# Optimization experiments

Hardware: AMD Instinct MI355X
Metric: run time of the kernel (lower is better)

## Reference

```python
import jax, jax.numpy as jnp
import numpy as np

D_MODEL = 1024
N_HEADS = 16
N_KV = 4
HEAD_DIM = D_MODEL // N_HEADS
B, T, CACHE_LEN = 2, 1024, 1024
MAX_SEQ = 4096
ROPE_BASE = 10000.0


def _rope_tables(max_seq_len=MAX_SEQ, head_dim=HEAD_DIM, base=ROPE_BASE):
    inv_freq = 1.0 / (base ** (np.arange(0, head_dim, 2, dtype=np.float32) / head_dim))
    t = np.arange(max_seq_len, dtype=np.float32)
    freqs = np.outer(t, inv_freq)                      # [S, hd/2]
    emb = np.concatenate([freqs, freqs], axis=-1)      # [S, hd]
    return jnp.asarray(np.cos(emb)), jnp.asarray(np.sin(emb))


def _rotate_half(x):
    x1, x2 = jnp.split(x, 2, axis=-1)
    return jnp.concatenate([-x2, x1], axis=-1)


def setup_inputs() -> dict:
    key = jax.random.key(0)
    ks = jax.random.split(key, 8)
    return {
        "x": jax.random.normal(ks[0], (B, T, D_MODEL), dtype=jnp.float32),
        "k_cache": jax.random.normal(ks[1], (B, N_KV, CACHE_LEN, HEAD_DIM), dtype=jnp.float32),
        "v_cache": jax.random.normal(ks[2], (B, N_KV, CACHE_LEN, HEAD_DIM), dtype=jnp.float32),
        "position_indices": jax.random.randint(ks[3], (B, T), 0, 1024, dtype=jnp.int32),
        "Wq": jax.random.normal(ks[4], (D_MODEL, D_MODEL), dtype=jnp.float32) * 0.02,
        "Wk": jax.random.normal(ks[5], (D_MODEL, N_KV * HEAD_DIM), dtype=jnp.float32) * 0.02,
        "Wv": jax.random.normal(ks[6], (D_MODEL, N_KV * HEAD_DIM), dtype=jnp.float32) * 0.02,
        "Wo": jax.random.normal(ks[7], (D_MODEL, D_MODEL), dtype=jnp.float32) * 0.02,
    }


def reference(x, k_cache, v_cache, position_indices, Wq, Wk, Wv, Wo):
    Bq, Tq, C = x.shape
    n_kv, cache_len, hd = k_cache.shape[1], k_cache.shape[2], k_cache.shape[3]
    n_heads = Wq.shape[1] // hd
    n_rep = n_heads // n_kv
    scale = hd ** -0.5

    cos, sin = _rope_tables()

    # projections -> [B, H, T, hd]
    q = (x @ Wq).reshape(Bq, Tq, n_heads, hd).transpose(0, 2, 1, 3)
    k = (x @ Wk).reshape(Bq, Tq, n_kv, hd).transpose(0, 2, 1, 3)
    v = (x @ Wv).reshape(Bq, Tq, n_kv, hd).transpose(0, 2, 1, 3)

    # progress-aware RoPE: position-indexed gather into tables, offset by cache len
    offset = cache_len
    t_seq = jnp.arange(Tq, dtype=jnp.int32)[None, :] + offset          # [1, T]
    idx = jnp.clip(position_indices.astype(jnp.int32) + t_seq, 0, cos.shape[0] - 1)  # [B, T]
    cos_b = cos[idx][:, None]  # [B, 1, T, hd]
    sin_b = sin[idx][:, None]
    q = q * cos_b + _rotate_half(q) * sin_b
    k = k * cos_b + _rotate_half(k) * sin_b

    # KV-cache concat
    k = jnp.concatenate([k_cache, k], axis=2)  # [B, n_kv, S, hd]
    v = jnp.concatenate([v_cache, v], axis=2)

    # GQA head expansion (repeat each kv head n_rep times, contiguous grouping)
    k_exp = jnp.repeat(k, n_rep, axis=1)  # [B, H, S, hd]
    v_exp = jnp.repeat(v, n_rep, axis=1)

    # manual attention path (k_cache provided -> NO causal mask, matching torch code)
    attn = jnp.einsum("bhtd,bhsd->bhts", q, k_exp) * scale
    attn = jax.nn.softmax(attn, axis=-1)
    out = jnp.einsum("bhts,bhsd->bhtd", attn, v_exp)
    out = out.transpose(0, 2, 1, 3).reshape(Bq, Tq, C)
    return out @ Wo, k, v
```

## Files before the change

kernel.cpp:

```cpp
#include <hip/hip_runtime.h>
#include <hip/hip_bf16.h>
#include <stdint.h>

#define D_MODEL 1024
#define N_HEADS 16
#define N_KV 4
#define HD 64
#define BB 2
#define TT 1024
#define CACHE_LEN 1024
#define SS 2048
#define MAX_SEQ 4096
#define QKV_N 1536
#define NROWS 32768
#define GRP_EL (SS * HD)
#define NSP 2

typedef __attribute__((ext_vector_type(8))) short bf16x8;
typedef __attribute__((ext_vector_type(4))) float f32x4;

__device__ inline short f2bs(float f) {
    __hip_bfloat16 h = __float2bfloat16(f);
    return *reinterpret_cast<short*>(&h);
}
__device__ inline float bs2f(short s) {
    return __uint_as_float((unsigned)(unsigned short)s << 16);
}

__device__ inline int kfrag_off(int s, int d) {
    return (s >> 4) * 1024 + ((d >= 32) ? 512 : 0) + ((((d & 31) >> 3) * 16 + (s & 15)) * 8) + (d & 7);
}
__device__ inline int vfrag_off(int s, int d) {
    return ((s >> 5) * 4 + (d >> 4)) * 512 + ((((s >> 2) & 3) * 16 + (d & 15)) * 8)
         + (((s >> 4) & 1) * 4) + (s & 3);
}

__device__ void transp_body(const float* __restrict__ src, short* __restrict__ dst,
                            int N, int bx, int by) {
    __shared__ short tile[32][34];
    int tx = threadIdx.x & 31, ty = threadIdx.x >> 5;
    int n0 = bx * 32, k0 = by * 32;
#pragma unroll
    for (int i = 0; i < 4; i++)
        tile[ty + i * 8][tx] = f2bs(src[(size_t)(k0 + ty + i * 8) * N + n0 + tx]);
    __syncthreads();
#pragma unroll
    for (int i = 0; i < 4; i++)
        dst[(size_t)(n0 + ty + i * 8) * 1024 + k0 + tx] = tile[tx][ty + i * 8];
}

__global__ void k_prep(const float* __restrict__ x, short* __restrict__ xb,
                       const float* __restrict__ Wq, const float* __restrict__ Wk,
                       const float* __restrict__ Wv, const float* __restrict__ Wo,
                       short* __restrict__ Wt, short* __restrict__ Wot,
                       const float* __restrict__ k_cache, const float* __restrict__ v_cache,
                       float* __restrict__ k_out, float* __restrict__ v_out,
                       short* __restrict__ kf, short* __restrict__ vf,
                       const int* __restrict__ pos,
                       float* __restrict__ costab, float* __restrict__ sintab) {
    int id = blockIdx.x;
    int g = threadIdx.x;
    if (id < 2048) {
        int i = (id * 256 + g) * 4;
        float4 v = *reinterpret_cast<const float4*>(x + i);
        short4 o = make_short4(f2bs(v.x), f2bs(v.y), f2bs(v.z), f2bs(v.w));
        *reinterpret_cast<short4*>(xb + i) = o;
        return;
    }
    id -= 2048;
    if (id < 1024) { transp_body(Wq, Wt, 1024, id & 31, id >> 5); return; }
    id -= 1024;
    if (id < 256)  { transp_body(Wk, Wt + (size_t)1024 * 1024, 256, id & 7, id >> 3); return; }
    id -= 256;
    if (id < 256)  { transp_body(Wv, Wt + (size_t)1280 * 1024, 256, id & 7, id >> 3); return; }
    id -= 256;
    if (id < 1024) { transp_body(Wo, Wot, 1024, id & 31, id >> 5); return; }
    id -= 1024;
    if (id < 2048) {
        int i = id * 256 + g;
        int d = i & 63;
        int s = (i >> 6) & 1023;
        int bh = i >> 16;
        size_t cidx = ((size_t)bh * CACHE_LEN + s) * HD + d;
        size_t oidx = ((size_t)bh * SS + s) * HD + d;
        float kv = k_cache[cidx];
        float vv = v_cache[cidx];
        k_out[oidx] = kv;
        v_out[oidx] = vv;
        kf[(size_t)bh * GRP_EL + kfrag_off(s, d)] = f2bs(kv);
        vf[(size_t)bh * GRP_EL + vfrag_off(s, d)] = f2bs(vv);
        return;
    }
    id -= 2048;
    {
        int p = id * 256 + g;
        int row = p >> 5, i = p & 31;
        int idx = pos[row] + (row & 1023) + CACHE_LEN;
        idx = min(max(idx, 0), MAX_SEQ - 1);
        float inv = expf(-(float)i * (9.210340371976184f / 32.0f));
        float sv, cv;
        sincosf((float)idx * inv, &sv, &cv);
        costab[p] = cv;
        sintab[p] = sv;
    }
}

__global__ __launch_bounds__(256) void k_gemm_qkv(
    const short* __restrict__ A, const short* __restrict__ Bt,
    const float* __restrict__ costab, const float* __restrict__ sintab,
    short* __restrict__ qb, short* __restrict__ kf, short* __restrict__ vf,
    float* __restrict__ k_out, float* __restrict__ v_out) {
    __shared__ float eplds[64 * 65];
    short* sA = (short*)eplds;
    short* sB = sA + 4096;
    int m0 = blockIdx.y * 64, n0 = blockIdx.x * 64;
    int g = threadIdx.x;
    int lane = g & 63, wave = g >> 6;
    int wr = wave >> 1, wc = wave & 1;
    int quad = lane >> 4, l15 = lane & 15;

    f32x4 acc[2][2] = {};

    for (int k0 = 0; k0 < 1024; k0 += 64) {
        __syncthreads();
#pragma unroll
        for (int i = 0; i < 2; i++) {
            int cb = wave * 2 + i;
            int h = cb >> 2, c = cb & 3;
            int row = c * 16 + (lane >> 2);
            int kcol = k0 + h * 32 + (lane & 3) * 8;
            const short* srcA = A + (size_t)(m0 + row) * 1024 + kcol;
            const short* srcB = Bt + (size_t)(n0 + row) * 1024 + kcol;
            __builtin_amdgcn_global_load_lds(
                (const __attribute__((address_space(1))) void*)srcA,
                (__attribute__((address_space(3))) void*)((char*)sA + h * 4096 + c * 1024), 16, 0, 0);
            __builtin_amdgcn_global_load_lds(
                (const __attribute__((address_space(1))) void*)srcB,
                (__attribute__((address_space(3))) void*)((char*)sB + h * 4096 + c * 1024), 16, 0, 0);
        }
        __syncthreads();
#pragma unroll
        for (int h = 0; h < 2; h++) {
            bf16x8 af[2], bfr[2];
#pragma unroll
            for (int i = 0; i < 2; i++)
                af[i] = *reinterpret_cast<const bf16x8*>(sA + h * 2048 + (wr * 32 + i * 16 + l15) * 32 + quad * 8);
#pragma unroll
            for (int j = 0; j < 2; j++)
                bfr[j] = *reinterpret_cast<const bf16x8*>(sB + h * 2048 + (wc * 32 + j * 16 + l15) * 32 + quad * 8);
#pragma unroll
            for (int i = 0; i < 2; i++)
#pragma unroll
                for (int j = 0; j < 2; j++)
                    acc[i][j] = __builtin_amdgcn_mfma_f32_16x16x32_bf16(af[i], bfr[j], acc[i][j], 0, 0, 0);
        }
    }
    __syncthreads();
#pragma unroll
    for (int i = 0; i < 2; i++)
#pragma unroll
        for (int j = 0; j < 2; j++)
#pragma unroll
            for (int r = 0; r < 4; r++)
                eplds[(wr * 32 + i * 16 + quad * 4 + r) * 65 + wc * 32 + j * 16 + l15] = acc[i][j][r];
    __syncthreads();

    int bx = blockIdx.x;
    const float QS = 0.18033688011112042f;
    if (bx < 20) {
#pragma unroll
        for (int rep = 0; rep < 8; rep++) {
            int p = rep * 256 + g;
            int row = p >> 5, i = p & 31;
            int m = m0 + row;
            int b = m >> 10, t = m & 1023;
            float cv = costab[m * 32 + i], sv = sintab[m * 32 + i];
            float x1 = eplds[row * 65 + i], x2 = eplds[row * 65 + i + 32];
            float o1 = x1 * cv - x2 * sv;
            float o2 = x2 * cv + x1 * sv;
            if (bx < 16) {
                size_t qbase = ((size_t)(b * N_HEADS + bx) * TT + t) * HD;
                qb[qbase + i]      = f2bs(o1 * QS);
                qb[qbase + i + 32] = f2bs(o2 * QS);
            } else {
                int h = bx - 16;
                int s = CACHE_LEN + t;
                size_t kbase = ((size_t)(b * N_KV + h) * SS + s) * HD;
                k_out[kbase + i]      = o1;
                k_out[kbase + i + 32] = o2;
                short* kfb = kf + (size_t)(b * N_KV + h) * GRP_EL;
                kfb[kfrag_off(s, i)]      = f2bs(o1);
                kfb[kfrag_off(s, i + 32)] = f2bs(o2);
            }
        }
    } else {
        int h = bx - 20;
#pragma unroll
        for (int rep = 0; rep < 16; rep++) {
            int p = rep * 256 + g;
            int row = p >> 6, d = p & 63;
            int m = m0 + row;
            int b = m >> 10, t = m & 1023;
            int s = CACHE_LEN + t;
            float val = eplds[row * 65 + d];
            v_out[((size_t)(b * N_KV + h) * SS + s) * HD + d] = val;
            vf[(size_t)(b * N_KV + h) * GRP_EL + vfrag_off(s, d)] = f2bs(val);
        }
    }
}

__global__ __launch_bounds__(256) void k_gemm64(
    const short* __restrict__ A, const short* __restrict__ Bt, float* __restrict__ C,
    int M, int N, int K) {
    __shared__ short sA[2][64 * 32];
    __shared__ short sB[2][64 * 32];
    int m0 = blockIdx.y * 64, n0 = blockIdx.x * 64;
    int g = threadIdx.x;
    int lane = g & 63, wave = g >> 6;
    int wr = wave >> 1, wc = wave & 1;
    int quad = lane >> 4, l15 = lane & 15;

    f32x4 acc[2][2] = {};

    for (int k0 = 0; k0 < K; k0 += 64) {
        __syncthreads();
#pragma unroll
        for (int i = 0; i < 2; i++) {
            int cb = wave * 2 + i;
            int h = cb >> 2, c = cb & 3;
            int row = c * 16 + (lane >> 2);
            int kcol = k0 + h * 32 + (lane & 3) * 8;
            const short* srcA = A + (size_t)(m0 + row) * K + kcol;
            const short* srcB = Bt + (size_t)(n0 + row) * K + kcol;
            __builtin_amdgcn_global_load_lds(
                (const __attribute__((address_space(1))) void*)srcA,
                (__attribute__((address_space(3))) void*)((char*)&sA[h][0] + c * 1024), 16, 0, 0);
            __builtin_amdgcn_global_load_lds(
                (const __attribute__((address_space(1))) void*)srcB,
                (__attribute__((address_space(3))) void*)((char*)&sB[h][0] + c * 1024), 16, 0, 0);
        }
        __syncthreads();
#pragma unroll
        for (int h = 0; h < 2; h++) {
            bf16x8 af[2], bfr[2];
#pragma unroll
            for (int i = 0; i < 2; i++)
                af[i] = *reinterpret_cast<const bf16x8*>(&sA[h][(wr * 32 + i * 16 + l15) * 32 + quad * 8]);
#pragma unroll
            for (int j = 0; j < 2; j++)
                bfr[j] = *reinterpret_cast<const bf16x8*>(&sB[h][(wc * 32 + j * 16 + l15) * 32 + quad * 8]);
#pragma unroll
            for (int i = 0; i < 2; i++)
#pragma unroll
                for (int j = 0; j < 2; j++)
                    acc[i][j] = __builtin_amdgcn_mfma_f32_16x16x32_bf16(af[i], bfr[j], acc[i][j], 0, 0, 0);
        }
    }
#pragma unroll
    for (int i = 0; i < 2; i++) {
        int m = m0 + wr * 32 + i * 16 + quad * 4;
#pragma unroll
        for (int j = 0; j < 2; j++) {
            int n = n0 + wc * 32 + j * 16 + l15;
#pragma unroll
            for (int r = 0; r < 4; r++)
                C[(size_t)(m + r) * N + n] = acc[i][j][r];
        }
    }
}

__global__ __launch_bounds__(256, 4) void k_attn(
    const short* __restrict__ qb, const short* __restrict__ kf, const short* __restrict__ vf,
    ushort* __restrict__ po, float* __restrict__ pl) {
    __shared__ short tile[8192];
    int bx = blockIdx.x;
    int sp = bx >> 5;
    int bh = bx & 31;
    int b = bh >> 4, h = bh & 15;
    int hkv = h >> 2;
    int lane = threadIdx.x & 63, wave = threadIdx.x >> 6;
    int quad = lane >> 4, l15 = lane & 15;
    int tw0 = blockIdx.y * 128 + wave * 16;
    int tw1 = tw0 + 64;

    const short* qrow0 = qb + ((size_t)bh * TT + tw0 + l15) * HD;
    const short* qrow1 = qb + ((size_t)bh * TT + tw1 + l15) * HD;
    bf16x8 aq00 = *reinterpret_cast<const bf16x8*>(qrow0 + quad * 8);
    bf16x8 aq01 = *reinterpret_cast<const bf16x8*>(qrow0 + 32 + quad * 8);
    bf16x8 aq10 = *reinterpret_cast<const bf16x8*>(qrow1 + quad * 8);
    bf16x8 aq11 = *reinterpret_cast<const bf16x8*>(qrow1 + 32 + quad * 8);

    const short* kfb = kf + (size_t)(b * N_KV + hkv) * GRP_EL;
    const short* vfb = vf + (size_t)(b * N_KV + hkv) * GRP_EL;

    f32x4 o0[4] = {}, o1[4] = {};
    float lr0 = 0.f, lr1 = 0.f;

    int sbeg = sp * (SS / NSP);
    for (int s0 = sbeg; s0 < sbeg + SS / NSP; s0 += 64) {
        __syncthreads();
#pragma unroll
        for (int i = 0; i < 4; i++) {
            int ch = wave * 4 + i;
            const short* src = (ch < 8)
                ? kfb + (s0 >> 4) * 1024 + ch * 512 + lane * 8
                : vfb + (s0 >> 5) * 2048 + (ch - 8) * 512 + lane * 8;
            __builtin_amdgcn_global_load_lds(
                (const __attribute__((address_space(1))) void*)src,
                (__attribute__((address_space(3))) void*)((char*)tile + ch * 1024), 16, 0, 0);
        }
        __syncthreads();

#pragma unroll
        for (int pp = 0; pp < 2; pp++) {
            f32x4 s0c[2], s1c[2];
#pragma unroll
            for (int ti = 0; ti < 2; ti++) {
                int nt = pp * 2 + ti;
                bf16x8 ak0 = *reinterpret_cast<const bf16x8*>(tile + nt * 1024 + lane * 8);
                bf16x8 ak1 = *reinterpret_cast<const bf16x8*>(tile + nt * 1024 + 512 + lane * 8);
                f32x4 z = {};
                z = __builtin_amdgcn_mfma_f32_16x16x32_bf16(ak0, aq00, z, 0, 0, 0);
                z = __builtin_amdgcn_mfma_f32_16x16x32_bf16(ak1, aq01, z, 0, 0, 0);
                s0c[ti] = z;
                f32x4 w = {};
                w = __builtin_amdgcn_mfma_f32_16x16x32_bf16(ak0, aq10, w, 0, 0, 0);
                w = __builtin_amdgcn_mfma_f32_16x16x32_bf16(ak1, aq11, w, 0, 0, 0);
                s1c[ti] = w;
            }
            bf16x8 bp0, bp1;
#pragma unroll
            for (int ti = 0; ti < 2; ti++)
#pragma unroll
                for (int r = 0; r < 4; r++) {
                    float p0 = exp2f(s0c[ti][r]);
                    float p1 = exp2f(s1c[ti][r]);
                    lr0 += p0;
                    lr1 += p1;
                    bp0[ti * 4 + r] = f2bs(p0);
                    bp1[ti * 4 + r] = f2bs(p1);
                }
#pragma unroll
            for (int dt = 0; dt < 4; dt++) {
                bf16x8 av = *reinterpret_cast<const bf16x8*>(
                    tile + 4096 + (pp * 4 + dt) * 512 + lane * 8);
                o0[dt] = __builtin_amdgcn_mfma_f32_16x16x32_bf16(av, bp0, o0[dt], 0, 0, 0);
                o1[dt] = __builtin_amdgcn_mfma_f32_16x16x32_bf16(av, bp1, o1[dt], 0, 0, 0);
            }
        }
    }

    lr0 += __shfl_xor(lr0, 16);
    lr0 += __shfl_xor(lr0, 32);
    lr1 += __shfl_xor(lr1, 16);
    lr1 += __shfl_xor(lr1, 32);

    size_t row0 = (size_t)bh * TT + tw0 + l15;
    size_t row1 = (size_t)bh * TT + tw1 + l15;
    if (quad == 0) {
        pl[(size_t)sp * NROWS + row0] = lr0;
        pl[(size_t)sp * NROWS + row1] = lr1;
    }
#pragma unroll
    for (int dt = 0; dt < 4; dt++) {
        ushort4 w0, w1;
        w0.x = (ushort)f2bs(o0[dt][0]); w0.y = (ushort)f2bs(o0[dt][1]);
        w0.z = (ushort)f2bs(o0[dt][2]); w0.w = (ushort)f2bs(o0[dt][3]);
        w1.x = (ushort)f2bs(o1[dt][0]); w1.y = (ushort)f2bs(o1[dt][1]);
        w1.z = (ushort)f2bs(o1[dt][2]); w1.w = (ushort)f2bs(o1[dt][3]);
        *reinterpret_cast<ushort4*>(po + ((size_t)sp * NROWS + row0) * 64 + dt * 16 + quad * 4) = w0;
        *reinterpret_cast<ushort4*>(po + ((size_t)sp * NROWS + row1) * 64 + dt * 16 + quad * 4) = w1;
    }
}

__global__ void k_merge(const ushort* __restrict__ po, const float* __restrict__ pl,
                        short* __restrict__ ob) {
    int g = threadIdx.x;
    int row = blockIdx.x * 16 + (g >> 4);
    int d0 = (g & 15) * 4;
    float l = 0.f;
#pragma unroll
    for (int sp = 0; sp < NSP; sp++) l += pl[(size_t)sp * NROWS + row];
    float a0 = 0, a1 = 0, a2 = 0, a3 = 0;
#pragma unroll
    for (int sp = 0; sp < NSP; sp++) {
        ushort4 u = *reinterpret_cast<const ushort4*>(po + ((size_t)sp * NROWS + row) * 64 + d0);
        a0 += __uint_as_float((unsigned)u.x << 16);
        a1 += __uint_as_float((unsigned)u.y << 16);
        a2 += __uint_as_float((unsigned)u.z << 16);
        a3 += __uint_as_float((unsigned)u.w << 16);
    }
    float inv = 1.0f / l;
    int bh = row >> 10, t = row & 1023;
    int b = bh >> 4, h = bh & 15;
    short4 w = make_short4(f2bs(a0 * inv), f2bs(a1 * inv), f2bs(a2 * inv), f2bs(a3 * inv));
    *reinterpret_cast<short4*>(ob + (size_t)(b * TT + t) * D_MODEL + h * 64 + d0) = w;
}

extern "C" void kernel_launch(void* const* d_in, const int* in_sizes, int n_in,
                              void* d_out, int out_size, void* d_ws, size_t ws_size,
                              hipStream_t stream) {
    (void)in_sizes; (void)n_in; (void)out_size; (void)ws_size;
    const float* x       = (const float*)d_in[0];
    const float* k_cache = (const float*)d_in[1];
    const float* v_cache = (const float*)d_in[2];
    const int*   pos     = (const int*)d_in[3];
    const float* Wq      = (const float*)d_in[4];
    const float* Wk      = (const float*)d_in[5];
    const float* Wv      = (const float*)d_in[6];
    const float* Wo      = (const float*)d_in[7];

    float* out   = (float*)d_out;
    float* k_out = out + (size_t)BB * TT * D_MODEL;
    float* v_out = k_out + (size_t)BB * N_KV * SS * HD;

    char* ws = (char*)d_ws;
    short* xb     = (short*)(ws);
    short* Wt     = (short*)(ws + (4u << 20));
    float* costab = (float*)(ws + (7u << 20));
    float* sintab = (float*)(ws + (7u << 20) + (256u << 10));
    short* qbuf   = (short*)(ws + (8u << 20));
    short* kfr    = (short*)(ws + (12u << 20));
    short* vfr    = (short*)(ws + (14u << 20));
    short* obuf   = (short*)(ws + (16u << 20));
    short* Wot    = (short*)(ws + (20u << 20));
    float* pl     = (float*)(ws + (22u << 20));
    ushort* po    = (ushort*)(ws);

    k_prep<<<6912, 256, 0, stream>>>(x, xb, Wq, Wk, Wv, Wo, Wt, Wot,
                                     k_cache, v_cache, k_out, v_out, kfr, vfr,
                                     pos, costab, sintab);

    k_gemm_qkv<<<dim3(QKV_N / 64, 2048 / 64), 256, 0, stream>>>(
        xb, Wt, costab, sintab, qbuf, kfr, vfr, k_out, v_out);

    k_attn<<<dim3(32 * NSP, TT / 128), 256, 0, stream>>>(qbuf, kfr, vfr, po, pl);
    k_merge<<<2048, 256, 0, stream>>>(po, pl, obuf);

    k_gemm64<<<dim3(1024 / 64, 2048 / 64), 256, 0, stream>>>(
        obuf, Wot, (float*)d_out, 2048, 1024, 1024);
}
```

Before: 149.4 us.

## Double-buffer LDS staging in GEMMs and attention, drop split-KV merge

Adds double-buffered LDS staging to the QKV GEMM, the output GEMM and the attention kernel, so the global-to-LDS copy of the next K/KV tile is issued before computing on the current tile. Each loop now needs one barrier per iteration instead of two. The attention kernel no longer splits the sequence into two halves with a separate merge kernel; it processes the full sequence per block and normalises and writes bf16 output directly. This removes a launch and the partial-result round trip, but halves the attention grid (256 blocks) and doubles LDS use per block, which may cut occupancy.

```diff
diff --git a/kernel.cpp b/kernel.cpp
--- a/kernel.cpp
+++ b/kernel.cpp
@@ -12,9 +12,7 @@
 #define SS 2048
 #define MAX_SEQ 4096
 #define QKV_N 1536
-#define NROWS 32768
 #define GRP_EL (SS * HD)
-#define NSP 2
 
 typedef __attribute__((ext_vector_type(8))) short bf16x8;
 typedef __attribute__((ext_vector_type(4))) float f32x4;
@@ -23,9 +21,10 @@
     __hip_bfloat16 h = __float2bfloat16(f);
     return *reinterpret_cast<short*>(&h);
 }
-__device__ inline float bs2f(short s) {
-    return __uint_as_float((unsigned)(unsigned short)s << 16);
-}
+
+#define GLDS(gp, lp) __builtin_amdgcn_global_load_lds( \
+    (const __attribute__((address_space(1))) void*)(gp), \
+    (__attribute__((address_space(3))) void*)(lp), 16, 0, 0)
 
 __device__ inline int kfrag_off(int s, int d) {
     return (s >> 4) * 1024 + ((d >= 32) ? 512 : 0) + ((((d & 31) >> 3) * 16 + (s & 15)) * 8) + (d & 7);
@@ -110,9 +109,10 @@
     const float* __restrict__ costab, const float* __restrict__ sintab,
     short* __restrict__ qb, short* __restrict__ kf, short* __restrict__ vf,
     float* __restrict__ k_out, float* __restrict__ v_out) {
-    __shared__ float eplds[64 * 65];
-    short* sA = (short*)eplds;
-    short* sB = sA + 4096;
+    __shared__ short smem[16384];
+    short* sA = smem;
+    short* sB = smem + 8192;
+    float* eplds = (float*)smem;
     int m0 = blockIdx.y * 64, n0 = blockIdx.x * 64;
     int g = threadIdx.x;
     int lane = g & 63, wave = g >> 6;
@@ -121,41 +121,48 @@
 
     f32x4 acc[2][2] = {};
 
+    int srow = (lane >> 2);
+    int scol = (lane & 3) * 8;
+#define STAGE_G(buf, k0)                                                              \
+    {                                                                                 \
+        _Pragma("unroll")                                                             \
+        for (int i = 0; i < 2; i++) {                                                 \
+            int cb = wave * 2 + i;                                                    \
+            int h = cb >> 2, c = cb & 3;                                              \
+            int row = c * 16 + srow;                                                  \
+            int kcol = (k0) + h * 32 + scol;                                          \
+            GLDS(A + (size_t)(m0 + row) * 1024 + kcol,                                \
+                 (char*)(sA + (buf) * 4096 + h * 2048) + c * 1024);                   \
+            GLDS(Bt + (size_t)(n0 + row) * 1024 + kcol,                               \
+                 (char*)(sB + (buf) * 4096 + h * 2048) + c * 1024);                   \
+        }                                                                             \
+    }
+
+    STAGE_G(0, 0);
+    __syncthreads();
+    int buf = 0;
     for (int k0 = 0; k0 < 1024; k0 += 64) {
-        __syncthreads();
-#pragma unroll
-        for (int i = 0; i < 2; i++) {
-            int cb = wave * 2 + i;
-            int h = cb >> 2, c = cb & 3;
-            int row = c * 16 + (lane >> 2);
-            int kcol = k0 + h * 32 + (lane & 3) * 8;
-            const short* srcA = A + (size_t)(m0 + row) * 1024 + kcol;
-            const short* srcB = Bt + (size_t)(n0 + row) * 1024 + kcol;
-            __builtin_amdgcn_global_load_lds(
-                (const __attribute__((address_space(1))) void*)srcA,
-                (__attribute__((address_space(3))) void*)((char*)sA + h * 4096 + c * 1024), 16, 0, 0);
-            __builtin_amdgcn_global_load_lds(
-                (const __attribute__((address_space(1))) void*)srcB,
-                (__attribute__((address_space(3))) void*)((char*)sB + h * 4096 + c * 1024), 16, 0, 0);
-        }
-        __syncthreads();
+        if (k0 + 64 < 1024) STAGE_G(buf ^ 1, k0 + 64);
 #pragma unroll
         for (int h = 0; h < 2; h++) {
             bf16x8 af[2], bfr[2];
 #pragma unroll
             for (int i = 0; i < 2; i++)
-                af[i] = *reinterpret_cast<const bf16x8*>(sA + h * 2048 + (wr * 32 + i * 16 + l15) * 32 + quad * 8);
+                af[i] = *reinterpret_cast<const bf16x8*>(
+                    sA + buf * 4096 + h * 2048 + (wr * 32 + i * 16 + l15) * 32 + quad * 8);
 #pragma unroll
             for (int j = 0; j < 2; j++)
-                bfr[j] = *reinterpret_cast<const bf16x8*>(sB + h * 2048 + (wc * 32 + j * 16 + l15) * 32 + quad * 8);
+                bfr[j] = *reinterpret_cast<const bf16x8*>(
+                    sB + buf * 4096 + h * 2048 + (wc * 32 + j * 16 + l15) * 32 + quad * 8);
 #pragma unroll
             for (int i = 0; i < 2; i++)
 #pragma unroll
                 for (int j = 0; j < 2; j++)
                     acc[i][j] = __builtin_amdgcn_mfma_f32_16x16x32_bf16(af[i], bfr[j], acc[i][j], 0, 0, 0);
         }
-    }
-    __syncthreads();
+        __syncthreads();
+        buf ^= 1;
+    }
 #pragma unroll
     for (int i = 0; i < 2; i++)
 #pragma unroll
@@ -212,8 +219,8 @@
 __global__ __launch_bounds__(256) void k_gemm64(
     const short* __restrict__ A, const short* __restrict__ Bt, float* __restrict__ C,
     int M, int N, int K) {
-    __shared__ short sA[2][64 * 32];
-    __shared__ short sB[2][64 * 32];
+    __shared__ short sA[2][2][2048];
+    __shared__ short sB[2][2][2048];
     int m0 = blockIdx.y * 64, n0 = blockIdx.x * 64;
     int g = threadIdx.x;
     int lane = g & 63, wave = g >> 6;
@@ -221,40 +228,42 @@
     int quad = lane >> 4, l15 = lane & 15;
 
     f32x4 acc[2][2] = {};
-
+    int srow = (lane >> 2);
+    int scol = (lane & 3) * 8;
+#define STAGE_W(buf, k0)                                                             \
+    {                                                                                \
+        _Pragma("unroll")                                                            \
+        for (int i = 0; i < 2; i++) {                                                \
+            int cb = wave * 2 + i;                                                   \
+            int h = cb >> 2, c = cb & 3;                                             \
+            int row = c * 16 + srow;                                                 \
+            int kcol = (k0) + h * 32 + scol;                                         \
+            GLDS(A + (size_t)(m0 + row) * K + kcol, (char*)&sA[buf][h][0] + c * 1024);\
+            GLDS(Bt + (size_t)(n0 + row) * K + kcol, (char*)&sB[buf][h][0] + c * 1024);\
+        }                                                                            \
+    }
+    STAGE_W(0, 0);
+    __syncthreads();
+    int buf = 0;
     for (int k0 = 0; k0 < K; k0 += 64) {
-        __syncthreads();
-#pragma unroll
-        for (int i = 0; i < 2; i++) {
-            int cb = wave * 2 + i;
-            int h = cb >> 2, c = cb & 3;
-            int row = c * 16 + (lane >> 2);
-            int kcol = k0 + h * 32 + (lane & 3) * 8;
-            const short* srcA = A + (size_t)(m0 + row) * K + kcol;
-            const short* srcB = Bt + (size_t)(n0 + row) * K + kcol;
-            __builtin_amdgcn_global_load_lds(
-                (const __attribute__((address_space(1))) void*)srcA,
-                (__attribute__((address_space(3))) void*)((char*)&sA[h][0] + c * 1024), 16, 0, 0);
-            __builtin_amdgcn_global_load_lds(
-                (const __attribute__((address_space(1))) void*)srcB,
-                (__attribute__((address_space(3))) void*)((char*)&sB[h][0] + c * 1024), 16, 0, 0);
-        }
-        __syncthreads();
+        if (k0 + 64 < K) STAGE_W(buf ^ 1, k0 + 64);
 #pragma unroll
         for (int h = 0; h < 2; h++) {
             bf16x8 af[2], bfr[2];
 #pragma unroll
             for (int i = 0; i < 2; i++)
-                af[i] = *reinterpret_cast<const bf16x8*>(&sA[h][(wr * 32 + i * 16 + l15) * 32 + quad * 8]);
+                af[i] = *reinterpret_cast<const bf16x8*>(&sA[buf][h][(wr * 32 + i * 16 + l15) * 32 + quad * 8]);
 #pragma unroll
             for (int j = 0; j < 2; j++)
-                bfr[j] = *reinterpret_cast<const bf16x8*>(&sB[h][(wc * 32 + j * 16 + l15) * 32 + quad * 8]);
+                bfr[j] = *reinterpret_cast<const bf16x8*>(&sB[buf][h][(wc * 32 + j * 16 + l15) * 32 + quad * 8]);
 #pragma unroll
             for (int i = 0; i < 2; i++)
 #pragma unroll
                 for (int j = 0; j < 2; j++)
                     acc[i][j] = __builtin_amdgcn_mfma_f32_16x16x32_bf16(af[i], bfr[j], acc[i][j], 0, 0, 0);
         }
+        __syncthreads();
+        buf ^= 1;
     }
 #pragma unroll
     for (int i = 0; i < 2; i++) {
@@ -271,11 +280,9 @@
 
 __global__ __launch_bounds__(256, 4) void k_attn(
     const short* __restrict__ qb, const short* __restrict__ kf, const short* __restrict__ vf,
-    ushort* __restrict__ po, float* __restrict__ pl) {
-    __shared__ short tile[8192];
-    int bx = blockIdx.x;
-    int sp = bx >> 5;
-    int bh = bx & 31;
+    short* __restrict__ ob) {
+    __shared__ short tile[2][8192];
+    int bh = blockIdx.x;
     int b = bh >> 4, h = bh & 15;
     int hkv = h >> 2;
     int lane = threadIdx.x & 63, wave = threadIdx.x >> 6;
@@ -296,29 +303,32 @@
     f32x4 o0[4] = {}, o1[4] = {};
     float lr0 = 0.f, lr1 = 0.f;
 
-    int sbeg = sp * (SS / NSP);
-    for (int s0 = sbeg; s0 < sbeg + SS / NSP; s0 += 64) {
-        __syncthreads();
-#pragma unroll
-        for (int i = 0; i < 4; i++) {
-            int ch = wave * 4 + i;
-            const short* src = (ch < 8)
-                ? kfb + (s0 >> 4) * 1024 + ch * 512 + lane * 8
-                : vfb + (s0 >> 5) * 2048 + (ch - 8) * 512 + lane * 8;
-            __builtin_amdgcn_global_load_lds(
-                (const __attribute__((address_space(1))) void*)src,
-                (__attribute__((address_space(3))) void*)((char*)tile + ch * 1024), 16, 0, 0);
-        }
-        __syncthreads();
-
+#define STAGE_KV(bufi, s0)                                                    \
+    {                                                                         \
+        _Pragma("unroll")                                                     \
+        for (int i = 0; i < 4; i++) {                                         \
+            int ch = wave * 4 + i;                                            \
+            const short* src = (ch < 8)                                       \
+                ? kfb + ((s0) >> 4) * 1024 + ch * 512 + lane * 8              \
+                : vfb + ((s0) >> 5) * 2048 + (ch - 8) * 512 + lane * 8;       \
+            GLDS(src, (char*)&tile[bufi][0] + ch * 1024);                     \
+        }                                                                     \
+    }
+
+    STAGE_KV(0, 0);
+    __syncthreads();
+    int buf = 0;
+    for (int s0 = 0; s0 < SS; s0 += 64) {
+        if (s0 + 64 < SS) STAGE_KV(buf ^ 1, s0 + 64);
+        const short* tb = &tile[buf][0];
 #pragma unroll
         for (int pp = 0; pp < 2; pp++) {
             f32x4 s0c[2], s1c[2];
 #pragma unroll
             for (int ti = 0; ti < 2; ti++) {
                 int nt = pp * 2 + ti;
-                bf16x8 ak0 = *reinterpret_cast<const bf16x8*>(tile + nt * 1024 + lane * 8);
-                bf16x8 ak1 = *reinterpret_cast<const bf16x8*>(tile + nt * 1024 + 512 + lane * 8);
+                bf16x8 ak0 = *reinterpret_cast<const bf16x8*>(tb + nt * 1024 + lane * 8);
+                bf16x8 ak1 = *reinterpret_cast<const bf16x8*>(tb + nt * 1024 + 512 + lane * 8);
                 f32x4 z = {};
                 z = __builtin_amdgcn_mfma_f32_16x16x32_bf16(ak0, aq00, z, 0, 0, 0);
                 z = __builtin_amdgcn_mfma_f32_16x16x32_bf16(ak1, aq01, z, 0, 0, 0);
@@ -343,58 +353,33 @@
 #pragma unroll
             for (int dt = 0; dt < 4; dt++) {
                 bf16x8 av = *reinterpret_cast<const bf16x8*>(
-                    tile + 4096 + (pp * 4 + dt) * 512 + lane * 8);
+                    tb + 4096 + (pp * 4 + dt) * 512 + lane * 8);
                 o0[dt] = __builtin_amdgcn_mfma_f32_16x16x32_bf16(av, bp0, o0[dt], 0, 0, 0);
                 o1[dt] = __builtin_amdgcn_mfma_f32_16x16x32_bf16(av, bp1, o1[dt], 0, 0, 0);
             }
         }
+        __syncthreads();
+        buf ^= 1;
     }
 
     lr0 += __shfl_xor(lr0, 16);
     lr0 += __shfl_xor(lr0, 32);
     lr1 += __shfl_xor(lr1, 16);
     lr1 += __shfl_xor(lr1, 32);
-
-    size_t row0 = (size_t)bh * TT + tw0 + l15;
-    size_t row1 = (size_t)bh * TT + tw1 + l15;
-    if (quad == 0) {
-        pl[(size_t)sp * NROWS + row0] = lr0;
-        pl[(size_t)sp * NROWS + row1] = lr1;
-    }
+    float inv0 = 1.0f / lr0;
+    float inv1 = 1.0f / lr1;
+
+    size_t row0 = (size_t)(b * TT) + tw0 + l15;
+    size_t row1 = (size_t)(b * TT) + tw1 + l15;
 #pragma unroll
     for (int dt = 0; dt < 4; dt++) {
-        ushort4 w0, w1;
-        w0.x = (ushort)f2bs(o0[dt][0]); w0.y = (ushort)f2bs(o0[dt][1]);
-        w0.z = (ushort)f2bs(o0[dt][2]); w0.w = (ushort)f2bs(o0[dt][3]);
-        w1.x = (ushort)f2bs(o1[dt][0]); w1.y = (ushort)f2bs(o1[dt][1]);
-        w1.z = (ushort)f2bs(o1[dt][2]); w1.w = (ushort)f2bs(o1[dt][3]);
-        *reinterpret_cast<ushort4*>(po + ((size_t)sp * NROWS + row0) * 64 + dt * 16 + quad * 4) = w0;
-        *reinterpret_cast<ushort4*>(po + ((size_t)sp * NROWS + row1) * 64 + dt * 16 + quad * 4) = w1;
-    }
-}
-
-__global__ void k_merge(const ushort* __restrict__ po, const float* __restrict__ pl,
-                        short* __restrict__ ob) {
-    int g = threadIdx.x;
-    int row = blockIdx.x * 16 + (g >> 4);
-    int d0 = (g & 15) * 4;
-    float l = 0.f;
-#pragma unroll
-    for (int sp = 0; sp < NSP; sp++) l += pl[(size_t)sp * NROWS + row];
-    float a0 = 0, a1 = 0, a2 = 0, a3 = 0;
-#pragma unroll
-    for (int sp = 0; sp < NSP; sp++) {
-        ushort4 u = *reinterpret_cast<const ushort4*>(po + ((size_t)sp * NROWS + row) * 64 + d0);
-        a0 += __uint_as_float((unsigned)u.x << 16);
-        a1 += __uint_as_float((unsigned)u.y << 16);
-        a2 += __uint_as_float((unsigned)u.z << 16);
-        a3 += __uint_as_float((unsigned)u.w << 16);
-    }
-    float inv = 1.0f / l;
-    int bh = row >> 10, t = row & 1023;
-    int b = bh >> 4, h = bh & 15;
-    short4 w = make_short4(f2bs(a0 * inv), f2bs(a1 * inv), f2bs(a2 * inv), f2bs(a3 * inv));
-    *reinterpret_cast<short4*>(ob + (size_t)(b * TT + t) * D_MODEL + h * 64 + d0) = w;
+        short4 w0 = make_short4(f2bs(o0[dt][0] * inv0), f2bs(o0[dt][1] * inv0),
+                                f2bs(o0[dt][2] * inv0), f2bs(o0[dt][3] * inv0));
+        short4 w1 = make_short4(f2bs(o1[dt][0] * inv1), f2bs(o1[dt][1] * inv1),
+                                f2bs(o1[dt][2] * inv1), f2bs(o1[dt][3] * inv1));
+        *reinterpret_cast<short4*>(ob + row0 * D_MODEL + h * 64 + dt * 16 + quad * 4) = w0;
+        *reinterpret_cast<short4*>(ob + row1 * D_MODEL + h * 64 + dt * 16 + quad * 4) = w1;
+    }
 }
 
 extern "C" void kernel_launch(void* const* d_in, const int* in_sizes, int n_in,
@@ -424,8 +409,6 @@
     short* vfr    = (short*)(ws + (14u << 20));
     short* obuf   = (short*)(ws + (16u << 20));
     short* Wot    = (short*)(ws + (20u << 20));
-    float* pl     = (float*)(ws + (22u << 20));
-    ushort* po    = (ushort*)(ws);
 
     k_prep<<<6912, 256, 0, stream>>>(x, xb, Wq, Wk, Wv, Wo, Wt, Wot,
                                      k_cache, v_cache, k_out, v_out, kfr, vfr,
@@ -434,8 +417,7 @@
     k_gemm_qkv<<<dim3(QKV_N / 64, 2048 / 64), 256, 0, stream>>>(
         xb, Wt, costab, sintab, qbuf, kfr, vfr, k_out, v_out);
 
-    k_attn<<<dim3(32 * NSP, TT / 128), 256, 0, stream>>>(qbuf, kfr, vfr, po, pl);
-    k_merge<<<2048, 256, 0, stream>>>(po, pl, obuf);
+    k_attn<<<dim3(32, TT / 128), 256, 0, stream>>>(qbuf, kfr, vfr, obuf);
 
     k_gemm64<<<dim3(1024 / 64, 2048 / 64), 256, 0, stream>>>(
         obuf, Wot, (float*)d_out, 2048, 1024, 1024);
```

Result: no change. 148.2 us (-0.8%).
